# Optimization experiments

Measured on AMD Instinct MI355X. Metric: run time of the kernel, lower is better.

The kernel has to match this reference:

```python
import jax, jax.numpy as jnp
import numpy as np

HEADS = 16
EMBED = 1024


def setup_inputs() -> dict:
    key = jax.random.key(0)
    k1, k2, k3, k4, k5, k6 = jax.random.split(key, 6)
    N, S, E = 2, 2048, EMBED
    return {
        "values": jax.random.normal(k1, (N, S, E), dtype=jnp.float32),
        "keys": jax.random.normal(k2, (N, S, E), dtype=jnp.float32),
        "query": jax.random.normal(k3, (N, S, E), dtype=jnp.float32),
        "mask": jax.random.randint(k4, (N, 1, S, S), 0, 2, dtype=jnp.int32),
        "W_out": jax.random.normal(k5, (E, E), dtype=jnp.float32) * 0.02,
        "b_out": jax.random.normal(k6, (E,), dtype=jnp.float32) * 0.02,
    }


def reference(values, keys, query, mask, W_out, b_out):
    N, Q, E = query.shape
    K = keys.shape[1]
    H = HEADS
    D = E // H
    v = values.reshape(N, K, H, D)
    k = keys.reshape(N, K, H, D)
    q = query.reshape(N, Q, H, D)
    # [N, H, Q, K] score matrix (faithful to the naive einsum formulation)
    energy = jnp.einsum("nqhd,nkhd->nhqk", q, k)
    energy = jnp.where(mask == 0, jnp.float32(-1e20), energy)
    # NOTE: original scales by sqrt(embed_size), not sqrt(head_dim)
    attention = jax.nn.softmax(energy / jnp.sqrt(jnp.float32(E)), axis=3)
    out = jnp.einsum("nhqk,nkhd->nqhd", attention, v).reshape(N, Q, E)
    return out @ W_out.T + b_out
```

## Files before the change

kernel.cpp:

```cpp
#include <hip/hip_runtime.h>
#include <hip/hip_bf16.h>


#define S_LEN  2048
#define EMB    1024
#define NHEAD  16
#define DHEAD  64
#define NBATCH 2

typedef float              f32x4    __attribute__((ext_vector_type(4)));
typedef __bf16             bf16x8   __attribute__((ext_vector_type(8)));
typedef unsigned short     ushort8v __attribute__((ext_vector_type(8)));
typedef unsigned long long u64;

union FragU { ushort8v u; bf16x8 b; };

__device__ __forceinline__ unsigned short f2b(float f) {
  union { __hip_bfloat16 h; unsigned short u; } c;
  c.h = __float2bfloat16(f);
  return c.u;
}

__device__ __forceinline__ unsigned int cvt_pk_bf16(float lo, float hi) {
  unsigned int r;
  asm("v_cvt_pk_bf16_f32 %0, %1, %2" : "=v"(r) : "v"(lo), "v"(hi));
  return r;
}

#define GLD16(g, l)                                                            \
  __builtin_amdgcn_global_load_lds(                                            \
      (__attribute__((address_space(1))) void*)(g),                            \
      (__attribute__((address_space(3))) void*)(l), 16, 0, 0)

__global__ __launch_bounds__(256) void prep(
    const float* __restrict__ Wo, unsigned short* __restrict__ Wb,
    const float* __restrict__ Kg, unsigned short* __restrict__ Kb,
    const float* __restrict__ Vg, unsigned short* __restrict__ Vt,
    const int* __restrict__ Mg,   u64* __restrict__ Mb)
{
  const int bid = blockIdx.x;
  const int tid = threadIdx.x;
  if (bid < 2560) {
    const float* X = (bid < 512) ? Wo : Kg;
    unsigned short* Y = (bid < 512) ? Wb : Kb;
    const int bb = (bid < 512) ? bid : bid - 512;
    const size_t i = ((size_t)bb * 256 + tid) * 8;
    float4 a = *reinterpret_cast<const float4*>(X + i);
    float4 b = *reinterpret_cast<const float4*>(X + i + 4);
    ushort8v u;
    u[0] = f2b(a.x); u[1] = f2b(a.y); u[2] = f2b(a.z); u[3] = f2b(a.w);
    u[4] = f2b(b.x); u[5] = f2b(b.y); u[6] = f2b(b.z); u[7] = f2b(b.w);
    *reinterpret_cast<ushort8v*>(Y + i) = u;
  } else if (bid < 3584) {
    __shared__ unsigned short T[64][72];
    const int b2 = bid - 2560;
    const int sb = b2 & 31, h = (b2 >> 5) & 15, n = b2 >> 9;
    const int r = tid >> 2, cb = (tid & 3) * 16;
    const float* src = Vg + ((size_t)(n * S_LEN + sb * 64 + r)) * EMB + h * DHEAD + cb;
    ushort8v u0, u1;
#pragma unroll
    for (int j = 0; j < 2; ++j) {
      float4 x = *reinterpret_cast<const float4*>(src + j * 4);
      u0[j*4+0] = f2b(x.x); u0[j*4+1] = f2b(x.y); u0[j*4+2] = f2b(x.z); u0[j*4+3] = f2b(x.w);
      float4 y = *reinterpret_cast<const float4*>(src + 8 + j * 4);
      u1[j*4+0] = f2b(y.x); u1[j*4+1] = f2b(y.y); u1[j*4+2] = f2b(y.z); u1[j*4+3] = f2b(y.w);
    }
    *reinterpret_cast<ushort8v*>(&T[r][cb])     = u0;
    *reinterpret_cast<ushort8v*>(&T[r][cb + 8]) = u1;
    __syncthreads();
    const int d = tid >> 2, sc_ = (tid & 3) * 16;
    ushort8v o0, o1;
#pragma unroll
    for (int j = 0; j < 8; ++j) { o0[j] = T[sc_ + j][d]; o1[j] = T[sc_ + 8 + j][d]; }
    unsigned short* dst = Vt + ((size_t)((n * NHEAD + h) * DHEAD + d)) * S_LEN + sb * 64 + sc_;
    *reinterpret_cast<ushort8v*>(dst)     = o0;
    *reinterpret_cast<ushort8v*>(dst + 8) = o1;
  } else {
    const int b3 = bid - 3584;
    const size_t base = (size_t)b3 * 1024 + (tid >> 6) * 256;
    const int l = tid & 63;
#pragma unroll
    for (int j = 0; j < 4; ++j) {
      const int v = Mg[base + j * 64 + l];
      u64 bj = __ballot(v != 0);
      if (l == 0) Mb[base / 64 + j] = bj;
    }
  }
}

#define KBASE 0
#define VBASE 16384
#define PBASE 32768

__global__ __launch_bounds__(512, 4) void attn_fwd(
    const unsigned short* __restrict__ Kb,
    const unsigned short* __restrict__ Vtg,
    const float* __restrict__ Qg,
    const u64* __restrict__ Mbit,
    unsigned short* __restrict__ Og)
{
  __shared__ __attribute__((aligned(16))) char SMEM[49152];

  const int bid = blockIdx.x;
  const int qb = bid & 15, h = (bid >> 4) & 15, n = bid >> 8;
  const int nh = n * NHEAD + h;
  const int tid = threadIdx.x;
  const int w = tid >> 6, sp = w >> 2, wq = w & 3;
  const int l = tid & 63, lg = l >> 4, li = l & 15;
  const int lg4 = lg * 4;
  const int q0w = qb * 128 + wq * 32;

  FragU qf[2][2];
#pragma unroll
  for (int g = 0; g < 2; ++g) {
    const float* qp = Qg + (size_t)(n * S_LEN + q0w + g * 16 + li) * EMB + h * DHEAD + lg * 8;
#pragma unroll
    for (int s = 0; s < 2; ++s) {
      float4 a = *reinterpret_cast<const float4*>(qp + s * 32);
      float4 b = *reinterpret_cast<const float4*>(qp + s * 32 + 4);
      ushort8v u;
      u[0] = f2b(a.x); u[1] = f2b(a.y); u[2] = f2b(a.z); u[3] = f2b(a.w);
      u[4] = f2b(b.x); u[5] = f2b(b.y); u[6] = f2b(b.z); u[7] = f2b(b.w);
      qf[g][s].u = u;
    }
  }

  FragU ones;
#pragma unroll
  for (int j = 0; j < 8; ++j) ones.u[j] = 0x3F80;

  f32x4 acc[2][4];
#pragma unroll
  for (int g = 0; g < 2; ++g)
#pragma unroll
    for (int c = 0; c < 4; ++c) acc[g][c] = (f32x4){0.f, 0.f, 0.f, 0.f};
  f32x4 lacc[2];
  lacc[0] = (f32x4){0.f, 0.f, 0.f, 0.f};
  lacc[1] = (f32x4){0.f, 0.f, 0.f, 0.f};

  const int t = tid & 255;
  const int krow = t >> 3;
  const char* kbase = (const char*)Kb +
      ((size_t)n * S_LEN + sp * 1024 + krow) * (EMB * 2) + h * 128 +
      (((t & 7) * 16) ^ ((krow & 7) << 4));
  const int vrow = t >> 2;
  const char* vbase = (const char*)Vtg +
      ((size_t)nh * DHEAD + vrow) * (S_LEN * 2) + sp * 2048 +
      (((t & 3) * 16) ^ ((vrow & 3) << 4));

  const int rsw  = (li & 7) << 4;
  const int vrsw = (li & 3) << 4;
  const int psw  = (li & 3) << 4;

  char* Kme = SMEM + KBASE + sp * 4096;
  char* Vme = SMEM + VBASE + sp * 4096;
  char* Pw  = SMEM + PBASE + w * 2048;

  const u64* Mq0 = Mbit + ((size_t)n * S_LEN + q0w + li) * 32 + sp * 16;
  const u64* Mq1 = Mq0 + 16 * 32;

#define ATTN_STAGE(BUF, IT) do {                                               \
    GLD16(kbase + (size_t)(IT) * (32 * 2048), Kme + (BUF) * 8192 + t * 16);    \
    GLD16(vbase + (size_t)(IT) * 64,          Vme + (BUF) * 8192 + t * 16);    \
  } while (0)

#define ATTN_TILE(BUF, IT) do {                                                \
    __syncthreads();                                                           \
    if ((IT) + 1 < 32) ATTN_STAGE((BUF) ^ 1, (IT) + 1);                        \
    const u64 m0_ = Mq0[(IT) >> 1];                                            \
    const u64 m1_ = Mq1[(IT) >> 1];                                            \
    const unsigned int h0_ = ((IT) & 1) ? (unsigned int)(m0_ >> 32) : (unsigned int)m0_; \
    const unsigned int h1_ = ((IT) & 1) ? (unsigned int)(m1_ >> 32) : (unsigned int)m1_; \
    unsigned int nib_[2][2];                                                   \
    nib_[0][0] = h0_ >> lg4;  nib_[0][1] = h0_ >> (16 + lg4);                  \
    nib_[1][0] = h1_ >> lg4;  nib_[1][1] = h1_ >> (16 + lg4);                  \
    f32x4 sc_[2][2];                                                           \
    __builtin_amdgcn_s_setprio(1);                                             \
    _Pragma("unroll") for (int cc = 0; cc < 2; ++cc) {                         \
      FragU kf0_, kf1_;                                                        \
      kf0_.u = *reinterpret_cast<const ushort8v*>(                             \
          Kme + (BUF) * 8192 + ((cc * 16 + li) * 128 + ((lg * 16) ^ rsw)));    \
      kf1_.u = *reinterpret_cast<const ushort8v*>(                             \
          Kme + (BUF) * 8192 + ((cc * 16 + li) * 128 + ((64 + lg * 16) ^ rsw))); \
      _Pragma("unroll") for (int g = 0; g < 2; ++g) {                          \
        f32x4 a_ = (f32x4){0.f, 0.f, 0.f, 0.f};                                \
        a_ = __builtin_amdgcn_mfma_f32_16x16x32_bf16(kf0_.b, qf[g][0].b, a_, 0, 0, 0); \
        a_ = __builtin_amdgcn_mfma_f32_16x16x32_bf16(kf1_.b, qf[g][1].b, a_, 0, 0, 0); \
        sc_[g][cc] = a_;                                                       \
      }                                                                        \
    }                                                                          \
    __builtin_amdgcn_s_setprio(0);                                             \
    _Pragma("unroll") for (int g = 0; g < 2; ++g) {                            \
      _Pragma("unroll") for (int cc = 0; cc < 2; ++cc) {                       \
        float p_[4];                                                           \
        _Pragma("unroll") for (int r = 0; r < 4; ++r) {                        \
          float t_ = __builtin_amdgcn_exp2f(                                   \
              __builtin_fmaf(sc_[g][cc][r], 0.04508422002778011f, -5.770780163555854f)); \
          p_[r] = (nib_[g][cc] & (1u << r)) ? t_ : 0.f;                        \
        }                                                                      \
        uint2 pk_;                                                             \
        pk_.x = cvt_pk_bf16(p_[0], p_[1]);                                     \
        pk_.y = cvt_pk_bf16(p_[2], p_[3]);                                     \
        *reinterpret_cast<uint2*>(Pw + (g * 16 + li) * 64 +                    \
                                  ((cc * 32 + lg * 8) ^ psw)) = pk_;           \
      }                                                                        \
    }                                                                          \
    FragU pf_[2];                                                              \
    pf_[0].u = *reinterpret_cast<const ushort8v*>(Pw + li * 64 + ((lg * 16) ^ psw));        \
    pf_[1].u = *reinterpret_cast<const ushort8v*>(Pw + (16 + li) * 64 + ((lg * 16) ^ psw)); \
    __builtin_amdgcn_s_setprio(1);                                             \
    lacc[0] = __builtin_amdgcn_mfma_f32_16x16x32_bf16(pf_[0].b, ones.b, lacc[0], 0, 0, 0); \
    lacc[1] = __builtin_amdgcn_mfma_f32_16x16x32_bf16(pf_[1].b, ones.b, lacc[1], 0, 0, 0); \
    _Pragma("unroll") for (int c = 0; c < 4; ++c) {                            \
      FragU vf_;                                                               \
      vf_.u = *reinterpret_cast<const ushort8v*>(                              \
          Vme + (BUF) * 8192 + ((c * 16 + li) * 64 + ((lg * 16) ^ vrsw)));     \
      acc[0][c] = __builtin_amdgcn_mfma_f32_16x16x32_bf16(pf_[0].b, vf_.b, acc[0][c], 0, 0, 0); \
      acc[1][c] = __builtin_amdgcn_mfma_f32_16x16x32_bf16(pf_[1].b, vf_.b, acc[1][c], 0, 0, 0); \
    }                                                                          \
    __builtin_amdgcn_s_setprio(0);                                             \
  } while (0)

  ATTN_STAGE(0, 0);
  for (int it = 0; it < 32; it += 2) {
    ATTN_TILE(0, it);
    ATTN_TILE(1, it + 1);
  }

  __syncthreads();
  if (sp == 1) {
#pragma unroll
    for (int g = 0; g < 2; ++g)
#pragma unroll
      for (int c = 0; c < 4; ++c)
        *reinterpret_cast<f32x4*>(SMEM + wq * 8192 + l * 128 +
                                  ((g * 64 + c * 16) ^ ((l & 7) << 4))) = acc[g][c];
    *reinterpret_cast<f32x4*>(SMEM + PBASE + w * 2048 + l * 32)      = lacc[0];
    *reinterpret_cast<f32x4*>(SMEM + PBASE + w * 2048 + l * 32 + 16) = lacc[1];
  }
  __syncthreads();
  if (sp == 0) {
    f32x4 pl[2];
    pl[0] = *reinterpret_cast<const f32x4*>(SMEM + PBASE + (w + 4) * 2048 + l * 32);
    pl[1] = *reinterpret_cast<const f32x4*>(SMEM + PBASE + (w + 4) * 2048 + l * 32 + 16);
#pragma unroll
    for (int g = 0; g < 2; ++g) {
      float rin[4];
#pragma unroll
      for (int r = 0; r < 4; ++r) rin[r] = 1.0f / (lacc[g][r] + pl[g][r]);
#pragma unroll
      for (int c = 0; c < 4; ++c) {
        f32x4 pa = *reinterpret_cast<const f32x4*>(
            SMEM + wq * 8192 + l * 128 + ((g * 64 + c * 16) ^ ((l & 7) << 4)));
#pragma unroll
        for (int r = 0; r < 4; ++r) {
          const int qg_ = q0w + g * 16 + lg * 4 + r;
          Og[(size_t)(n * S_LEN + qg_) * EMB + h * DHEAD + c * 16 + li] =
              f2b((acc[g][c][r] + pa[r]) * rin[r]);
        }
      }
    }
  }
}

__global__ __launch_bounds__(256) void out_proj(
    const unsigned short* __restrict__ A,
    const unsigned short* __restrict__ W,
    const float* __restrict__ bias,
    float* __restrict__ Y)
{
  __shared__ __attribute__((aligned(16))) unsigned short At[2][8192];
  __shared__ __attribute__((aligned(16))) unsigned short Bt[2][4096];

  const int bid = blockIdx.x;
  const int nb = bid & 15, mb = bid >> 4;
  const int tid = threadIdx.x;
  const int w = tid >> 6, l = tid & 63, lg = l >> 4, li = l & 15;
  const int m0 = mb * 128, n0 = nb * 64;

  f32x4 acc[2][4];
#pragma unroll
  for (int g = 0; g < 2; ++g)
#pragma unroll
    for (int c = 0; c < 4; ++c) acc[g][c] = (f32x4){0.f, 0.f, 0.f, 0.f};

  const int srow8  = tid >> 3;
  const int schunk = (tid & 7) * 16;
  const int ssw    = (srow8 & 7) << 4;
  const char* abase = (const char*)A + ((size_t)m0 + srow8) * (EMB * 2) + (schunk ^ ssw);
  const char* bbase = (const char*)W + ((size_t)n0 + srow8) * (EMB * 2) + (schunk ^ ssw);
  const int rsw = (li & 7) << 4;

#define PROJ_STAGE(BUF, KK) do {                                               \
    const char* ab_ = abase + (KK) * 128;                                      \
    const char* bb_ = bbase + (KK) * 128;                                      \
    GLD16(ab_,             (char*)At + (BUF) * 16384 + w * 1024);              \
    GLD16(ab_ + 32 * 2048, (char*)At + (BUF) * 16384 + 4096 + w * 1024);       \
    GLD16(ab_ + 64 * 2048, (char*)At + (BUF) * 16384 + 8192 + w * 1024);       \
    GLD16(ab_ + 96 * 2048, (char*)At + (BUF) * 16384 + 12288 + w * 1024);      \
    GLD16(bb_,             (char*)Bt + (BUF) * 8192 + w * 1024);               \
    GLD16(bb_ + 32 * 2048, (char*)Bt + (BUF) * 8192 + 4096 + w * 1024);        \
  } while (0)

#define PROJ_TILE(BUF, KK) do {                                                \
    __syncthreads();                                                           \
    if ((KK) + 1 < 16) PROJ_STAGE((BUF) ^ 1, (KK) + 1);                        \
    __builtin_amdgcn_s_setprio(1);                                             \
    _Pragma("unroll") for (int s = 0; s < 2; ++s) {                            \
      FragU af_[2];                                                            \
      _Pragma("unroll") for (int g = 0; g < 2; ++g)                            \
        af_[g].u = *reinterpret_cast<const ushort8v*>(                         \
            (char*)At + (BUF) * 16384 +                                        \
            ((w * 32 + g * 16 + li) * 128 + ((s * 64 + lg * 16) ^ rsw)));      \
      _Pragma("unroll") for (int c = 0; c < 4; ++c) {                          \
        FragU bf_;                                                             \
        bf_.u = *reinterpret_cast<const ushort8v*>(                            \
            (char*)Bt + (BUF) * 8192 +                                         \
            ((c * 16 + li) * 128 + ((s * 64 + lg * 16) ^ rsw)));               \
        acc[0][c] = __builtin_amdgcn_mfma_f32_16x16x32_bf16(af_[0].b, bf_.b, acc[0][c], 0, 0, 0); \
        acc[1][c] = __builtin_amdgcn_mfma_f32_16x16x32_bf16(af_[1].b, bf_.b, acc[1][c], 0, 0, 0); \
      }                                                                        \
    }                                                                          \
    __builtin_amdgcn_s_setprio(0);                                             \
  } while (0)

  PROJ_STAGE(0, 0);
  for (int kk = 0; kk < 16; kk += 2) {
    PROJ_TILE(0, kk);
    PROJ_TILE(1, kk + 1);
  }

#pragma unroll
  for (int g = 0; g < 2; ++g)
#pragma unroll
    for (int c = 0; c < 4; ++c) {
      const float bv = bias[n0 + c * 16 + li];
#pragma unroll
      for (int r = 0; r < 4; ++r) {
        const int row = m0 + w * 32 + g * 16 + lg * 4 + r;
        Y[(size_t)row * EMB + n0 + c * 16 + li] = acc[g][c][r] + bv;
      }
    }
}

extern "C" void kernel_launch(void* const* d_in, const int* in_sizes, int n_in,
                              void* d_out, int out_size, void* d_ws, size_t ws_size,
                              hipStream_t stream) {
  const float* Vg = (const float*)d_in[0];
  const float* Kg = (const float*)d_in[1];
  const float* Qg = (const float*)d_in[2];
  const int*   Mg = (const int*)d_in[3];
  const float* Wo = (const float*)d_in[4];
  const float* bo = (const float*)d_in[5];
  float* Y = (float*)d_out;

  char* ws = (char*)d_ws;
  unsigned short* Og   = (unsigned short*)(ws);
  unsigned short* Wb   = (unsigned short*)(ws + (8u << 20));
  unsigned short* Kb16 = (unsigned short*)(ws + (10u << 20));
  unsigned short* Vt   = (unsigned short*)(ws + (18u << 20));
  u64*            Mbit = (u64*)(ws + (26u << 20));

  hipLaunchKernelGGL(prep, dim3(11776), dim3(256), 0, stream,
                     Wo, Wb, Kg, Kb16, Vg, Vt, Mg, Mbit);
  hipLaunchKernelGGL(attn_fwd, dim3(NBATCH * NHEAD * (S_LEN / 128)), dim3(512), 0, stream,
                     Kb16, Vt, Qg, Mbit, Og);
  hipLaunchKernelGGL(out_proj, dim3((NBATCH * S_LEN / 128) * (EMB / 64)), dim3(256), 0, stream,
                     Og, Wb, bo, Y);
}
```

Baseline: 103.0 us.

## Rewrite attention inner loop with 32x32 MFMA and register-resident P via permlane swap

Switches the attention kernel from 16x16x32 MFMAs to 32x32x16 MFMAs, computing S transposed so the probability tile stays in registers. A v_permlane32_swap rearranges it into the B-operand layout, which removes the per-tile LDS round trip for P. The row sum is now accumulated in scalar registers instead of through an extra MFMA against a ones vector. The key tile grows to 64 keys per iteration with 16 iterations, and LDS grows to 64KB. That may lower occupancy under the 4-blocks-per-CU launch bound and raises register pressure from the f32x16 accumulators.

```diff
diff --git a/kernel.cpp b/kernel.cpp
--- a/kernel.cpp
+++ b/kernel.cpp
@@ -9,11 +9,13 @@
 #define NBATCH 2
 
 typedef float              f32x4    __attribute__((ext_vector_type(4)));
+typedef float              f32x16   __attribute__((ext_vector_type(16)));
 typedef __bf16             bf16x8   __attribute__((ext_vector_type(8)));
 typedef unsigned short     ushort8v __attribute__((ext_vector_type(8)));
 typedef unsigned long long u64;
 
 union FragU { ushort8v u; bf16x8 b; };
+union BFrag { unsigned u32[4]; bf16x8 b; };
 
 __device__ __forceinline__ unsigned short f2b(float f) {
   union { __hip_bfloat16 h; unsigned short u; } c;
@@ -26,6 +28,8 @@
   asm("v_cvt_pk_bf16_f32 %0, %1, %2" : "=v"(r) : "v"(lo), "v"(hi));
   return r;
 }
+
+#define PSWAP(a, b) asm("v_permlane32_swap_b32 %0, %1" : "+v"(a), "+v"(b))
 
 #define GLD16(g, l)                                                            \
   __builtin_amdgcn_global_load_lds(                                            \
@@ -88,10 +92,6 @@
   }
 }
 
-#define KBASE 0
-#define VBASE 16384
-#define PBASE 32768
-
 __global__ __launch_bounds__(512, 4) void attn_fwd(
     const unsigned short* __restrict__ Kb,
     const unsigned short* __restrict__ Vtg,
@@ -99,165 +99,152 @@
     const u64* __restrict__ Mbit,
     unsigned short* __restrict__ Og)
 {
-  __shared__ __attribute__((aligned(16))) char SMEM[49152];
+  __shared__ __attribute__((aligned(16))) char SMEM[65536];
 
   const int bid = blockIdx.x;
   const int qb = bid & 15, h = (bid >> 4) & 15, n = bid >> 8;
   const int nh = n * NHEAD + h;
   const int tid = threadIdx.x;
   const int w = tid >> 6, sp = w >> 2, wq = w & 3;
-  const int l = tid & 63, lg = l >> 4, li = l & 15;
-  const int lg4 = lg * 4;
+  const int l = tid & 63, q5 = l & 31, hi = l >> 5;
+  const int hi4 = hi * 4;
   const int q0w = qb * 128 + wq * 32;
-
-  FragU qf[2][2];
-#pragma unroll
-  for (int g = 0; g < 2; ++g) {
-    const float* qp = Qg + (size_t)(n * S_LEN + q0w + g * 16 + li) * EMB + h * DHEAD + lg * 8;
-#pragma unroll
-    for (int s = 0; s < 2; ++s) {
-      float4 a = *reinterpret_cast<const float4*>(qp + s * 32);
-      float4 b = *reinterpret_cast<const float4*>(qp + s * 32 + 4);
+  const int qg = q0w + q5;
+
+  FragU qf[4];
+  {
+    const float* qp = Qg + ((size_t)(n * S_LEN + qg)) * EMB + h * DHEAD + hi * 8;
+#pragma unroll
+    for (int s = 0; s < 4; ++s) {
+      float4 a = *reinterpret_cast<const float4*>(qp + s * 16);
+      float4 b = *reinterpret_cast<const float4*>(qp + s * 16 + 4);
       ushort8v u;
       u[0] = f2b(a.x); u[1] = f2b(a.y); u[2] = f2b(a.z); u[3] = f2b(a.w);
       u[4] = f2b(b.x); u[5] = f2b(b.y); u[6] = f2b(b.z); u[7] = f2b(b.w);
-      qf[g][s].u = u;
-    }
-  }
-
-  FragU ones;
-#pragma unroll
-  for (int j = 0; j < 8; ++j) ones.u[j] = 0x3F80;
-
-  f32x4 acc[2][4];
-#pragma unroll
-  for (int g = 0; g < 2; ++g)
-#pragma unroll
-    for (int c = 0; c < 4; ++c) acc[g][c] = (f32x4){0.f, 0.f, 0.f, 0.f};
-  f32x4 lacc[2];
-  lacc[0] = (f32x4){0.f, 0.f, 0.f, 0.f};
-  lacc[1] = (f32x4){0.f, 0.f, 0.f, 0.f};
-
-  const int t = tid & 255;
-  const int krow = t >> 3;
+      qf[s].u = u;
+    }
+  }
+
+  f32x16 acc0 = {}, acc1 = {};
+  float rsum = 0.f;
+
+  const int t8 = tid & 255;
+  const int srow = t8 >> 3, sc = t8 & 7;
   const char* kbase = (const char*)Kb +
-      ((size_t)n * S_LEN + sp * 1024 + krow) * (EMB * 2) + h * 128 +
-      (((t & 7) * 16) ^ ((krow & 7) << 4));
-  const int vrow = t >> 2;
+      ((size_t)(n * S_LEN + sp * 1024 + srow)) * 2048 + h * 128 +
+      ((sc * 16) ^ ((srow & 7) << 4));
   const char* vbase = (const char*)Vtg +
-      ((size_t)nh * DHEAD + vrow) * (S_LEN * 2) + sp * 2048 +
-      (((t & 3) * 16) ^ ((vrow & 3) << 4));
-
-  const int rsw  = (li & 7) << 4;
-  const int vrsw = (li & 3) << 4;
-  const int psw  = (li & 3) << 4;
-
-  char* Kme = SMEM + KBASE + sp * 4096;
-  char* Vme = SMEM + VBASE + sp * 4096;
-  char* Pw  = SMEM + PBASE + w * 2048;
-
-  const u64* Mq0 = Mbit + ((size_t)n * S_LEN + q0w + li) * 32 + sp * 16;
-  const u64* Mq1 = Mq0 + 16 * 32;
+      ((size_t)(nh * DHEAD + srow)) * 4096 + sp * 2048 +
+      ((sc * 16) ^ ((srow & 7) << 4));
+
+  char* Ksp = SMEM + sp * 16384;
+  char* Vsp = SMEM + 32768 + sp * 16384;
+  const int fsw = (l & 7) << 4;
+
+  const u64* Mq = Mbit + ((size_t)(n * S_LEN + qg)) * 32 + sp * 16;
 
 #define ATTN_STAGE(BUF, IT) do {                                               \
-    GLD16(kbase + (size_t)(IT) * (32 * 2048), Kme + (BUF) * 8192 + t * 16);    \
-    GLD16(vbase + (size_t)(IT) * 64,          Vme + (BUF) * 8192 + t * 16);    \
+    GLD16(kbase + (size_t)(IT) * 131072,          Ksp + (BUF) * 8192 + t8 * 16); \
+    GLD16(kbase + (size_t)(IT) * 131072 + 65536,  Ksp + (BUF) * 8192 + 4096 + t8 * 16); \
+    GLD16(vbase + (size_t)(IT) * 128,             Vsp + (BUF) * 8192 + t8 * 16); \
+    GLD16(vbase + (size_t)(IT) * 128 + 131072,    Vsp + (BUF) * 8192 + 4096 + t8 * 16); \
   } while (0)
 
 #define ATTN_TILE(BUF, IT) do {                                                \
     __syncthreads();                                                           \
-    if ((IT) + 1 < 32) ATTN_STAGE((BUF) ^ 1, (IT) + 1);                        \
-    const u64 m0_ = Mq0[(IT) >> 1];                                            \
-    const u64 m1_ = Mq1[(IT) >> 1];                                            \
-    const unsigned int h0_ = ((IT) & 1) ? (unsigned int)(m0_ >> 32) : (unsigned int)m0_; \
-    const unsigned int h1_ = ((IT) & 1) ? (unsigned int)(m1_ >> 32) : (unsigned int)m1_; \
-    unsigned int nib_[2][2];                                                   \
-    nib_[0][0] = h0_ >> lg4;  nib_[0][1] = h0_ >> (16 + lg4);                  \
-    nib_[1][0] = h1_ >> lg4;  nib_[1][1] = h1_ >> (16 + lg4);                  \
-    f32x4 sc_[2][2];                                                           \
-    __builtin_amdgcn_s_setprio(1);                                             \
-    _Pragma("unroll") for (int cc = 0; cc < 2; ++cc) {                         \
-      FragU kf0_, kf1_;                                                        \
-      kf0_.u = *reinterpret_cast<const ushort8v*>(                             \
-          Kme + (BUF) * 8192 + ((cc * 16 + li) * 128 + ((lg * 16) ^ rsw)));    \
-      kf1_.u = *reinterpret_cast<const ushort8v*>(                             \
-          Kme + (BUF) * 8192 + ((cc * 16 + li) * 128 + ((64 + lg * 16) ^ rsw))); \
-      _Pragma("unroll") for (int g = 0; g < 2; ++g) {                          \
-        f32x4 a_ = (f32x4){0.f, 0.f, 0.f, 0.f};                                \
-        a_ = __builtin_amdgcn_mfma_f32_16x16x32_bf16(kf0_.b, qf[g][0].b, a_, 0, 0, 0); \
-        a_ = __builtin_amdgcn_mfma_f32_16x16x32_bf16(kf1_.b, qf[g][1].b, a_, 0, 0, 0); \
-        sc_[g][cc] = a_;                                                       \
+    if ((IT) + 1 < 16) ATTN_STAGE((BUF) ^ 1, (IT) + 1);                        \
+    const u64 mrow_ = Mq[(IT)];                                                \
+    _Pragma("unroll") for (int b = 0; b < 2; ++b) {                            \
+      f32x16 Sb = {};                                                          \
+      __builtin_amdgcn_s_setprio(1);                                           \
+      _Pragma("unroll") for (int s = 0; s < 4; ++s) {                          \
+        FragU kf_;                                                             \
+        kf_.u = *reinterpret_cast<const ushort8v*>(                            \
+            Ksp + (BUF) * 8192 + ((b * 32 + q5) * 128 + ((s * 32 + hi * 16) ^ fsw))); \
+        Sb = __builtin_amdgcn_mfma_f32_32x32x16_bf16(kf_.b, qf[s].b, Sb, 0, 0, 0); \
       }                                                                        \
+      __builtin_amdgcn_s_setprio(0);                                           \
+      const unsigned m32_ = b ? (unsigned)(mrow_ >> 32) : (unsigned)mrow_;     \
+      float p_[16];                                                            \
+      _Pragma("unroll") for (int t = 0; t < 4; ++t) {                          \
+        const unsigned nib_ = m32_ >> (8 * t + hi4);                           \
+        _Pragma("unroll") for (int e = 0; e < 4; ++e) {                        \
+          const int r = 4 * t + e;                                             \
+          float ex_ = __builtin_amdgcn_exp2f(                                  \
+              __builtin_fmaf(Sb[r], 0.04508422002778011f, -5.770780163555854f)); \
+          p_[r] = ((nib_ >> e) & 1u) ? ex_ : 0.f;                              \
+          rsum += p_[r];                                                       \
+        }                                                                      \
+      }                                                                        \
+      unsigned U0 = cvt_pk_bf16(p_[0],  p_[1]),  U1 = cvt_pk_bf16(p_[2],  p_[3]); \
+      unsigned U2 = cvt_pk_bf16(p_[4],  p_[5]),  U3 = cvt_pk_bf16(p_[6],  p_[7]); \
+      unsigned U4 = cvt_pk_bf16(p_[8],  p_[9]),  U5 = cvt_pk_bf16(p_[10], p_[11]); \
+      unsigned U6 = cvt_pk_bf16(p_[12], p_[13]), U7 = cvt_pk_bf16(p_[14], p_[15]); \
+      PSWAP(U0, U2); PSWAP(U1, U3); PSWAP(U4, U6); PSWAP(U5, U7);              \
+      BFrag F0, F1;                                                            \
+      F0.u32[0] = U0; F0.u32[1] = U1; F0.u32[2] = U2; F0.u32[3] = U3;          \
+      F1.u32[0] = U4; F1.u32[1] = U5; F1.u32[2] = U6; F1.u32[3] = U7;          \
+      __builtin_amdgcn_s_setprio(1);                                           \
+      _Pragma("unroll") for (int db = 0; db < 2; ++db) {                       \
+        FragU vf0_, vf1_;                                                      \
+        vf0_.u = *reinterpret_cast<const ushort8v*>(                           \
+            Vsp + (BUF) * 8192 + ((db * 32 + q5) * 128 + (((2 * b) * 32 + hi * 16) ^ fsw))); \
+        vf1_.u = *reinterpret_cast<const ushort8v*>(                           \
+            Vsp + (BUF) * 8192 + ((db * 32 + q5) * 128 + (((2 * b + 1) * 32 + hi * 16) ^ fsw))); \
+        if (db == 0) {                                                         \
+          acc0 = __builtin_amdgcn_mfma_f32_32x32x16_bf16(vf0_.b, F0.b, acc0, 0, 0, 0); \
+          acc0 = __builtin_amdgcn_mfma_f32_32x32x16_bf16(vf1_.b, F1.b, acc0, 0, 0, 0); \
+        } else {                                                               \
+          acc1 = __builtin_amdgcn_mfma_f32_32x32x16_bf16(vf0_.b, F0.b, acc1, 0, 0, 0); \
+          acc1 = __builtin_amdgcn_mfma_f32_32x32x16_bf16(vf1_.b, F1.b, acc1, 0, 0, 0); \
+        }                                                                      \
+      }                                                                        \
+      __builtin_amdgcn_s_setprio(0);                                           \
     }                                                                          \
-    __builtin_amdgcn_s_setprio(0);                                             \
-    _Pragma("unroll") for (int g = 0; g < 2; ++g) {                            \
-      _Pragma("unroll") for (int cc = 0; cc < 2; ++cc) {                       \
-        float p_[4];                                                           \
-        _Pragma("unroll") for (int r = 0; r < 4; ++r) {                        \
-          float t_ = __builtin_amdgcn_exp2f(                                   \
-              __builtin_fmaf(sc_[g][cc][r], 0.04508422002778011f, -5.770780163555854f)); \
-          p_[r] = (nib_[g][cc] & (1u << r)) ? t_ : 0.f;                        \
-        }                                                                      \
-        uint2 pk_;                                                             \
-        pk_.x = cvt_pk_bf16(p_[0], p_[1]);                                     \
-        pk_.y = cvt_pk_bf16(p_[2], p_[3]);                                     \
-        *reinterpret_cast<uint2*>(Pw + (g * 16 + li) * 64 +                    \
-                                  ((cc * 32 + lg * 8) ^ psw)) = pk_;           \
-      }                                                                        \
-    }                                                                          \
-    FragU pf_[2];                                                              \
-    pf_[0].u = *reinterpret_cast<const ushort8v*>(Pw + li * 64 + ((lg * 16) ^ psw));        \
-    pf_[1].u = *reinterpret_cast<const ushort8v*>(Pw + (16 + li) * 64 + ((lg * 16) ^ psw)); \
-    __builtin_amdgcn_s_setprio(1);                                             \
-    lacc[0] = __builtin_amdgcn_mfma_f32_16x16x32_bf16(pf_[0].b, ones.b, lacc[0], 0, 0, 0); \
-    lacc[1] = __builtin_amdgcn_mfma_f32_16x16x32_bf16(pf_[1].b, ones.b, lacc[1], 0, 0, 0); \
-    _Pragma("unroll") for (int c = 0; c < 4; ++c) {                            \
-      FragU vf_;                                                               \
-      vf_.u = *reinterpret_cast<const ushort8v*>(                              \
-          Vme + (BUF) * 8192 + ((c * 16 + li) * 64 + ((lg * 16) ^ vrsw)));     \
-      acc[0][c] = __builtin_amdgcn_mfma_f32_16x16x32_bf16(pf_[0].b, vf_.b, acc[0][c], 0, 0, 0); \
-      acc[1][c] = __builtin_amdgcn_mfma_f32_16x16x32_bf16(pf_[1].b, vf_.b, acc[1][c], 0, 0, 0); \
-    }                                                                          \
-    __builtin_amdgcn_s_setprio(0);                                             \
   } while (0)
 
   ATTN_STAGE(0, 0);
-  for (int it = 0; it < 32; it += 2) {
+  for (int it = 0; it < 16; it += 2) {
     ATTN_TILE(0, it);
     ATTN_TILE(1, it + 1);
   }
 
+  const float rs = rsum + __shfl_xor(rsum, 32);
+
   __syncthreads();
   if (sp == 1) {
 #pragma unroll
-    for (int g = 0; g < 2; ++g)
-#pragma unroll
-      for (int c = 0; c < 4; ++c)
-        *reinterpret_cast<f32x4*>(SMEM + wq * 8192 + l * 128 +
-                                  ((g * 64 + c * 16) ^ ((l & 7) << 4))) = acc[g][c];
-    *reinterpret_cast<f32x4*>(SMEM + PBASE + w * 2048 + l * 32)      = lacc[0];
-    *reinterpret_cast<f32x4*>(SMEM + PBASE + w * 2048 + l * 32 + 16) = lacc[1];
+    for (int i = 0; i < 4; ++i) {
+      f32x4 v0 = (f32x4){acc0[4*i], acc0[4*i+1], acc0[4*i+2], acc0[4*i+3]};
+      f32x4 v1 = (f32x4){acc1[4*i], acc1[4*i+1], acc1[4*i+2], acc1[4*i+3]};
+      *reinterpret_cast<f32x4*>(SMEM + wq * 8192 + l * 128 + i * 16)      = v0;
+      *reinterpret_cast<f32x4*>(SMEM + wq * 8192 + l * 128 + 64 + i * 16) = v1;
+    }
+    *reinterpret_cast<float*>(SMEM + 32768 + wq * 256 + l * 4) = rs;
   }
   __syncthreads();
   if (sp == 0) {
-    f32x4 pl[2];
-    pl[0] = *reinterpret_cast<const f32x4*>(SMEM + PBASE + (w + 4) * 2048 + l * 32);
-    pl[1] = *reinterpret_cast<const f32x4*>(SMEM + PBASE + (w + 4) * 2048 + l * 32 + 16);
-#pragma unroll
-    for (int g = 0; g < 2; ++g) {
-      float rin[4];
-#pragma unroll
-      for (int r = 0; r < 4; ++r) rin[r] = 1.0f / (lacc[g][r] + pl[g][r]);
-#pragma unroll
-      for (int c = 0; c < 4; ++c) {
+    const float ors = *reinterpret_cast<const float*>(SMEM + 32768 + wq * 256 + l * 4);
+    const float rin = 1.0f / (rs + ors);
+    unsigned short* orow = Og + ((size_t)(n * S_LEN + qg)) * EMB + h * DHEAD + hi4;
+#pragma unroll
+    for (int db = 0; db < 2; ++db) {
+#pragma unroll
+      for (int t = 0; t < 4; ++t) {
         f32x4 pa = *reinterpret_cast<const f32x4*>(
-            SMEM + wq * 8192 + l * 128 + ((g * 64 + c * 16) ^ ((l & 7) << 4)));
-#pragma unroll
-        for (int r = 0; r < 4; ++r) {
-          const int qg_ = q0w + g * 16 + lg * 4 + r;
-          Og[(size_t)(n * S_LEN + qg_) * EMB + h * DHEAD + c * 16 + li] =
-              f2b((acc[g][c][r] + pa[r]) * rin[r]);
+            SMEM + wq * 8192 + l * 128 + db * 64 + t * 16);
+        float a0, a1, a2, a3;
+        if (db == 0) {
+          a0 = (acc0[4*t]   + pa[0]) * rin; a1 = (acc0[4*t+1] + pa[1]) * rin;
+          a2 = (acc0[4*t+2] + pa[2]) * rin; a3 = (acc0[4*t+3] + pa[3]) * rin;
+        } else {
+          a0 = (acc1[4*t]   + pa[0]) * rin; a1 = (acc1[4*t+1] + pa[1]) * rin;
+          a2 = (acc1[4*t+2] + pa[2]) * rin; a3 = (acc1[4*t+3] + pa[3]) * rin;
         }
+        uint2 pk;
+        pk.x = cvt_pk_bf16(a0, a1);
+        pk.y = cvt_pk_bf16(a2, a3);
+        *reinterpret_cast<uint2*>(orow + db * 32 + t * 8) = pk;
       }
     }
   }
```

Result: faster. 96.03 us (-6.8%).
